# Kernel optimization log

Measured on AMD Instinct MI355X. Metric: run time of the kernel, lower is better.

## Reference

```python
import jax, jax.numpy as jnp
import numpy as np

B, T, D, H = 4, 2048, 1024, 16
HD = D // H  # head_dim = 64

def setup_inputs() -> dict:
    key = jax.random.key(0)
    k1, k2, k3 = jax.random.split(key, 3)
    s = 1.0 / np.sqrt(D)
    x = jax.random.normal(k1, (B, T, D), dtype=jnp.float32)
    W_qkv = jax.random.normal(k2, (D, 3 * D), dtype=jnp.float32) * s
    W_proj = jax.random.normal(k3, (D, D), dtype=jnp.float32) * s
    return {"x": x, "W_qkv": W_qkv, "W_proj": W_proj}

def reference(x, W_qkv, W_proj):
    Bq, Tq, C = x.shape
    qkv = x @ W_qkv                                   # [B,T,3C]
    q, k, v = jnp.split(qkv, 3, axis=-1)
    def heads(t):  # [B,T,C] -> [B,H,T,HD]
        return t.reshape(Bq, Tq, H, HD).transpose(0, 2, 1, 3)
    q, k, v = heads(q), heads(k), heads(v)
    scale = 1.0 / np.sqrt(HD)
    att = jnp.einsum('bhqd,bhkd->bhqk', q, k) * scale  # [B,H,T,T]
    causal = jnp.tril(jnp.ones((Tq, Tq), dtype=bool))
    att = jnp.where(causal[None, None], att, -jnp.inf)
    att = jax.nn.softmax(att, axis=-1)
    y = jnp.einsum('bhqk,bhkd->bhqd', att, v)          # [B,H,T,HD]
    y = y.transpose(0, 2, 1, 3).reshape(Bq, Tq, C)
    return y @ W_proj
```

## Files before the change

kernel.cpp:

```cpp
#include <hip/hip_runtime.h>

typedef unsigned short ushort_t;
typedef __attribute__((ext_vector_type(8))) __bf16 bf16x8;
typedef __attribute__((ext_vector_type(4))) float f32x4;
typedef __attribute__((ext_vector_type(16))) float f32x16;
typedef __attribute__((ext_vector_type(4))) float float4v;
typedef __attribute__((ext_vector_type(8))) unsigned short ushort8v;
typedef __attribute__((ext_vector_type(4))) unsigned short ushort4v;
typedef __attribute__((ext_vector_type(4))) unsigned uint4v;

#define T_LEN 2048
#define D_DIM 1024
#define NHEAD 16
#define HDIM 64
#define BH 64
#define MROWS 8192
#define PERQKV ((size_t)BH * T_LEN * HDIM)

__device__ __forceinline__ ushort_t f2bf(float f) {
  unsigned u = __builtin_bit_cast(unsigned, f);
  u = (u + 0x7FFFu + ((u >> 16) & 1u)) >> 16;
  return (ushort_t)u;
}

__device__ __forceinline__ float fast_exp2(float x) {
  float r; asm("v_exp_f32 %0, %1" : "=v"(r) : "v"(x)); return r;
}

__device__ __forceinline__ void load_lds16(const ushort_t* g, ushort_t* l) {
  __builtin_amdgcn_global_load_lds((const __attribute__((address_space(1))) void*)g,
                                   (__attribute__((address_space(3))) void*)l, 16, 0, 0);
}

__global__ __launch_bounds__(256) void k_cvt_x(const float* __restrict__ x,
                                               ushort_t* __restrict__ xb) {
  int i = blockIdx.x * 256 + threadIdx.x;
  float4v v = ((const float4v*)x)[i];
  ushort4v o;
  o[0] = f2bf(v[0]); o[1] = f2bf(v[1]); o[2] = f2bf(v[2]); o[3] = f2bf(v[3]);
  ((ushort4v*)xb)[i] = o;
}

__global__ __launch_bounds__(256) void k_transpose(const float* __restrict__ W,
                                                   ushort_t* __restrict__ Wt,
                                                   int R, int C) {
  __shared__ ushort_t tile[32][33];
  int tx = threadIdx.x & 31, ty = threadIdx.x >> 5;
  int r0 = blockIdx.y << 5, c0 = blockIdx.x << 5;
#pragma unroll
  for (int i = 0; i < 4; ++i) {
    int r = ty + i * 8;
    tile[r][tx] = f2bf(W[(size_t)(r0 + r) * C + c0 + tx]);
  }
  __syncthreads();
#pragma unroll
  for (int i = 0; i < 4; ++i) {
    int r = ty + i * 8;
    Wt[(size_t)(c0 + r) * R + r0 + tx] = tile[tx][r];
  }
}

template <int N, int K, int EPI>
__global__ __launch_bounds__(256) void k_gemm(const ushort_t* __restrict__ A,
                                              const ushort_t* __restrict__ Bt,
                                              ushort_t* __restrict__ O16,
                                              float* __restrict__ O32) {
  __shared__ __align__(16) ushort_t Atile[128 * 32];
  __shared__ __align__(16) ushort_t Btile[128 * 32];
  const int tid = threadIdx.x;
  const int lane = tid & 63, w = tid >> 6;
  const int g = lane >> 4, c = lane & 15;
  const int wm = w >> 1, wn = w & 1;
  const int m0 = blockIdx.y * 128, n0 = blockIdx.x * 128;

  f32x4 acc[4][4];
#pragma unroll
  for (int i = 0; i < 4; ++i)
#pragma unroll
    for (int j = 0; j < 4; ++j) acc[i][j] = (f32x4){0.f, 0.f, 0.f, 0.f};

  for (int k0 = 0; k0 < K; k0 += 32) {
    __syncthreads();
#pragma unroll
    for (int r = 0; r < 2; ++r) {
      int flat = r * 256 + tid;
      int row = flat >> 2, slot = flat & 3;
      int gsl = slot ^ (row & 3);
      load_lds16(A + (size_t)(m0 + row) * K + k0 + gsl * 8,
                 &Atile[(r * 256 + w * 64) * 8]);
      load_lds16(Bt + (size_t)(n0 + row) * K + k0 + gsl * 8,
                 &Btile[(r * 256 + w * 64) * 8]);
    }
    __syncthreads();

    bf16x8 af[4], bfr[4];
#pragma unroll
    for (int mi = 0; mi < 4; ++mi) {
      int row = wm * 64 + mi * 16 + c;
      int sl = g ^ (row & 3);
      af[mi] = *(const bf16x8*)&Atile[row * 32 + sl * 8];
    }
#pragma unroll
    for (int ni = 0; ni < 4; ++ni) {
      int row = wn * 64 + ni * 16 + c;
      int sl = g ^ (row & 3);
      bfr[ni] = *(const bf16x8*)&Btile[row * 32 + sl * 8];
    }
#pragma unroll
    for (int mi = 0; mi < 4; ++mi)
#pragma unroll
      for (int ni = 0; ni < 4; ++ni)
        acc[mi][ni] = __builtin_amdgcn_mfma_f32_16x16x32_bf16(af[mi], bfr[ni],
                                                              acc[mi][ni], 0, 0, 0);
  }

#pragma unroll
  for (int mi = 0; mi < 4; ++mi)
#pragma unroll
    for (int ni = 0; ni < 4; ++ni) {
      int n = n0 + wn * 64 + ni * 16 + c;
#pragma unroll
      for (int j = 0; j < 4; ++j) {
        int m = m0 + wm * 64 + mi * 16 + g * 4 + j;
        float v = acc[mi][ni][j];
        if constexpr (EPI == 0) {
          int which = n >> 10, hn = n & 1023;
          int h = hn >> 6, d = hn & 63;
          int b = m >> 11, t = m & 2047;
          if (which == 0) v *= 0.18033688f;
          O16[(size_t)which * PERQKV +
              (((size_t)(b * NHEAD + h) * T_LEN + t) * HDIM + d)] = f2bf(v);
        } else {
          O32[(size_t)m * N + n] = v;
        }
      }
    }
}

__global__ __launch_bounds__(128, 4) void k_attn(const ushort_t* __restrict__ Q,
                                                 const ushort_t* __restrict__ Kv,
                                                 const ushort_t* __restrict__ Vv,
                                                 ushort_t* __restrict__ Y) {
  __shared__ __align__(16) ushort_t Kt[2][64 * 64];
  __shared__ __align__(16) ushort_t Vt[2][64 * 64];

  const int bid = blockIdx.x;
  const int bh = (bid & 7) * 8 + ((bid >> 3) & 7);
  const int pairidx = bid >> 6;
  const int pA = 31 - pairidx, pB = pairidx;
  const int nktA = pA + 1;
  const int total = nktA + pB + 1;

  const int tid = threadIdx.x, lane = tid & 63, w = tid >> 6;
  const int hi = lane >> 5, lc = lane & 31;
  const size_t base = (size_t)bh * (T_LEN * HDIM);

  int q32 = pA * 64 + w * 32;
  bf16x8 qf[4];
#pragma unroll
  for (int st = 0; st < 4; ++st)
    qf[st] = *(const bf16x8*)(Q + base + (size_t)(q32 + lc) * HDIM + st * 16 + hi * 8);

  f32x16 o0, o1;
#pragma unroll
  for (int i = 0; i < 16; ++i) { o0[i] = 0.f; o1[i] = 0.f; }
  float mrun = 0.f, lrun = 0.f;

  const int ksl = tid & 7, krow0 = tid >> 3;
  const int kpair = tid & 31, vk0 = 2 * kpair, vd0 = (tid >> 5) * 8;

  bf16x8 kreg[4];
  ushort8v vreg[4];
  auto stage_issue = [&](int kt) {
    const ushort_t* kb = Kv + base + (size_t)kt * 64 * HDIM;
    const ushort_t* vb = Vv + base + (size_t)kt * 64 * HDIM;
    vreg[0] = *(const ushort8v*)(vb + (size_t)vk0 * HDIM + vd0);
    vreg[1] = *(const ushort8v*)(vb + (size_t)(vk0 + 1) * HDIM + vd0);
    vreg[2] = *(const ushort8v*)(vb + (size_t)vk0 * HDIM + vd0 + 32);
    vreg[3] = *(const ushort8v*)(vb + (size_t)(vk0 + 1) * HDIM + vd0 + 32);
#pragma unroll
    for (int m = 0; m < 4; ++m)
      kreg[m] = *(const bf16x8*)(kb + (size_t)(krow0 + 16 * m) * HDIM + ksl * 8);
  };
  auto stage_write = [&](int buf) {
#pragma unroll
    for (int m = 0; m < 4; ++m) {
      int r = krow0 + 16 * m;
      *(bf16x8*)&Kt[buf][r * 64 + ((ksl ^ (r & 7)) << 3)] = kreg[m];
    }
#pragma unroll
    for (int e = 0; e < 8; ++e) {
      int rd = vd0 + e;
      unsigned pv = (unsigned)vreg[0][e] | ((unsigned)vreg[1][e] << 16);
      *(unsigned*)&Vt[buf][rd * 64 + (((kpair >> 2) ^ (rd & 7)) << 3) + 2 * (kpair & 3)] = pv;
      int rd2 = rd + 32;
      unsigned pv2 = (unsigned)vreg[2][e] | ((unsigned)vreg[3][e] << 16);
      *(unsigned*)&Vt[buf][rd2 * 64 + (((kpair >> 2) ^ (rd2 & 7)) << 3) + 2 * (kpair & 3)] = pv2;
    }
  };

  const int b_ = bh >> 4, h_ = bh & 15;
  auto epilogue = [&]() {
    float lt = lrun + __shfl_xor(lrun, 32);
    float invl = 1.f / lt;
#pragma unroll
    for (int r = 0; r < 16; ++r) {
      int cr = (r & 3) + 8 * (r >> 2) + 4 * hi;
      float iv = __shfl(invl, cr);
      size_t m = (size_t)b_ * T_LEN + q32 + cr;
      Y[m * D_DIM + h_ * HDIM + lc]      = f2bf(o0[r] * iv);
      Y[m * D_DIM + h_ * HDIM + 32 + lc] = f2bf(o1[r] * iv);
    }
  };

  stage_issue(0); stage_write(0);
  stage_issue(1);
  __syncthreads();

  for (int it = 0; it < total; ++it) {
    if (it == nktA) {
      epilogue();
      q32 = pB * 64 + w * 32;
#pragma unroll
      for (int st = 0; st < 4; ++st)
        qf[st] = *(const bf16x8*)(Q + base + (size_t)(q32 + lc) * HDIM + st * 16 + hi * 8);
#pragma unroll
      for (int i = 0; i < 16; ++i) { o0[i] = 0.f; o1[i] = 0.f; }
      mrun = 0.f; lrun = 0.f;
    }
    const int kt = (it < nktA) ? it : it - nktA;
    const int cur = it & 1;
    const ushort_t* kbuf = &Kt[cur][0];
    const ushort_t* vbuf = &Vt[cur][0];

    f32x16 s0, s1;
#pragma unroll
    for (int i = 0; i < 16; ++i) { s0[i] = 0.f; s1[i] = 0.f; }
    __builtin_amdgcn_s_setprio(1);
#pragma unroll
    for (int st = 0; st < 4; ++st) {
      bf16x8 kf0 = *(const bf16x8*)&kbuf[lc * 64 + (((2 * st + hi) ^ (lc & 7)) << 3)];
      s0 = __builtin_amdgcn_mfma_f32_32x32x16_bf16(kf0, qf[st], s0, 0, 0, 0);
    }
#pragma unroll
    for (int st = 0; st < 4; ++st) {
      bf16x8 kf1 = *(const bf16x8*)&kbuf[(32 + lc) * 64 + (((2 * st + hi) ^ (lc & 7)) << 3)];
      s1 = __builtin_amdgcn_mfma_f32_32x32x16_bf16(kf1, qf[st], s1, 0, 0, 0);
    }
    __builtin_amdgcn_s_setprio(0);

    if (kt * 64 + 63 > q32) {
      const int q = q32 + lc;
#pragma unroll
      for (int r = 0; r < 16; ++r) {
        int cr = (r & 3) + 8 * (r >> 2) + 4 * hi;
        if (kt * 64 + cr > q)      s0[r] = -3.0e38f;
        if (kt * 64 + 32 + cr > q) s1[r] = -3.0e38f;
      }
    }

    float tm[8];
#pragma unroll
    for (int i = 0; i < 8; ++i) tm[i] = fmaxf(fmaxf(s0[i], s0[i + 8]), fmaxf(s1[i], s1[i + 8]));
#pragma unroll
    for (int i = 0; i < 4; ++i) tm[i] = fmaxf(tm[i], tm[i + 4]);
    float tmax = fmaxf(fmaxf(tm[0], tm[1]), fmaxf(tm[2], tm[3]));
    tmax = fmaxf(tmax, __shfl_xor(tmax, 32));

    if (!__all(tmax <= mrun + 11.0f)) {
      float mnew = fmaxf(mrun, tmax);
      float sc = fast_exp2(mrun - mnew);
      lrun *= sc; mrun = mnew;
#pragma unroll
      for (int r = 0; r < 16; ++r) {
        int cr = (r & 3) + 8 * (r >> 2) + 4 * hi;
        float scr = __shfl(sc, cr);
        o0[r] *= scr; o1[r] *= scr;
      }
    }

#pragma unroll
    for (int r = 0; r < 16; ++r) s0[r] = fast_exp2(s0[r] - mrun);
#pragma unroll
    for (int r = 0; r < 16; ++r) s1[r] = fast_exp2(s1[r] - mrun);
    {
      float u0 = 0.f, u1 = 0.f, u2 = 0.f, u3 = 0.f;
#pragma unroll
      for (int i = 0; i < 4; ++i) {
        u0 += s0[i];     u1 += s0[i + 4];  u2 += s0[i + 8];  u3 += s0[i + 12];
        u0 += s1[i];     u1 += s1[i + 4];  u2 += s1[i + 8];  u3 += s1[i + 12];
      }
      lrun += (u0 + u1) + (u2 + u3);
    }

    unsigned wv[16];
#pragma unroll
    for (int i = 0; i < 8; ++i) {
      asm("v_cvt_pk_bf16_f32 %0, %1, %2" : "=v"(wv[i])     : "v"(s0[2 * i]), "v"(s0[2 * i + 1]));
      asm("v_cvt_pk_bf16_f32 %0, %1, %2" : "=v"(wv[8 + i]) : "v"(s1[2 * i]), "v"(s1[2 * i + 1]));
    }
    bf16x8 pf[4];
#pragma unroll
    for (int g4 = 0; g4 < 4; ++g4) {
      unsigned a0 = wv[4 * g4], a1 = wv[4 * g4 + 1];
      unsigned a2 = wv[4 * g4 + 2], a3 = wv[4 * g4 + 3];
      asm("v_permlane32_swap_b32 %0, %1" : "+v"(a0), "+v"(a2));
      asm("v_permlane32_swap_b32 %0, %1" : "+v"(a1), "+v"(a3));
      uint4v fw; fw[0] = a0; fw[1] = a1; fw[2] = a2; fw[3] = a3;
      pf[g4] = __builtin_bit_cast(bf16x8, fw);
    }

    __builtin_amdgcn_s_setprio(1);
#pragma unroll
    for (int km = 0; km < 4; ++km) {
      int gsl = ((2 * km + hi) ^ (lc & 7)) << 3;
      bf16x8 vb0 = *(const bf16x8*)&vbuf[lc * 64 + gsl];
      bf16x8 vb1 = *(const bf16x8*)&vbuf[(32 + lc) * 64 + gsl];
      o0 = __builtin_amdgcn_mfma_f32_32x32x16_bf16(pf[km], vb0, o0, 0, 0, 0);
      o1 = __builtin_amdgcn_mfma_f32_32x32x16_bf16(pf[km], vb1, o1, 0, 0, 0);
    }
    __builtin_amdgcn_s_setprio(0);

    if (it + 1 < total) stage_write((it + 1) & 1);
    if (it + 2 < total) {
      int itn = it + 2;
      stage_issue((itn < nktA) ? itn : itn - nktA);
    }
    __syncthreads();
  }

  epilogue();
}

extern "C" void kernel_launch(void* const* d_in, const int* in_sizes, int n_in,
                              void* d_out, int out_size, void* d_ws, size_t ws_size,
                              hipStream_t stream) {
  const float* x     = (const float*)d_in[0];
  const float* Wqkv  = (const float*)d_in[1];
  const float* Wproj = (const float*)d_in[2];
  float* out = (float*)d_out;
  ushort_t* ws = (ushort_t*)d_ws;

  ushort_t* Xb  = ws;
  ushort_t* WqT = Xb  + (size_t)MROWS * D_DIM;
  ushort_t* WpT = WqT + (size_t)3 * D_DIM * D_DIM;
  ushort_t* Qb  = WpT + (size_t)D_DIM * D_DIM;
  ushort_t* Kb  = Qb + PERQKV;
  ushort_t* Vb  = Kb + PERQKV;
  ushort_t* Yb  = Vb + PERQKV;

  k_cvt_x<<<(MROWS * D_DIM / 4) / 256, 256, 0, stream>>>(x, Xb);
  k_transpose<<<dim3(3 * D_DIM / 32, D_DIM / 32), 256, 0, stream>>>(Wqkv, WqT, D_DIM, 3 * D_DIM);
  k_transpose<<<dim3(D_DIM / 32, D_DIM / 32), 256, 0, stream>>>(Wproj, WpT, D_DIM, D_DIM);
  k_gemm<3 * D_DIM, D_DIM, 0><<<dim3(3 * D_DIM / 128, MROWS / 128), 256, 0, stream>>>(Xb, WqT, Qb, nullptr);
  k_attn<<<1024, 128, 0, stream>>>(Qb, Kb, Vb, Yb);
  k_gemm<D_DIM, D_DIM, 1><<<dim3(D_DIM / 128, MROWS / 128), 256, 0, stream>>>(Yb, WpT, nullptr, out);
}
```

Baseline: 189.1 us.

## Add larger-tile double-buffered QKV GEMM with swizzled LDS and XCD-aware block mapping

Replaces the 128x128 QKV projection GEMM with a dedicated 256x192-tile kernel using 512 threads, K-step of 64, double-buffered direct-to-LDS loads, XOR-swizzled shared-memory layout, and a block-index remap that groups tiles per XCD. It also raises MFMA issue priority around the compute loop. The goal is higher arithmetic intensity and overlap of global loads with MFMA work. The cost is heavier register and LDS use (two 80 KB-ish buffers), which may limit occupancy.

```diff
diff --git a/kernel.cpp b/kernel.cpp
--- a/kernel.cpp
+++ b/kernel.cpp
@@ -58,6 +58,94 @@
     int r = ty + i * 8;
     Wt[(size_t)(c0 + r) * R + r0 + tx] = tile[tx][r];
   }
+}
+
+__global__ __launch_bounds__(512, 2) void k_gemm1(const ushort_t* __restrict__ A,
+                                                  const ushort_t* __restrict__ Bt,
+                                                  ushort_t* __restrict__ O16) {
+  __shared__ __align__(16) ushort_t As[2][256 * 64];
+  __shared__ __align__(16) ushort_t Bs[2][192 * 64];
+  const int tid = threadIdx.x, lane = tid & 63, w = tid >> 6;
+  const int g = lane >> 4, c = lane & 15;
+  const int wm = w & 1, wn = w >> 1;
+  const int bid = blockIdx.x;
+  const int logical = (bid & 7) * 64 + (bid >> 3);
+  const int mb = logical & 31, nb = logical >> 5;
+  const int m0 = mb * 256, n0 = nb * 192;
+
+  const int strow = w * 8 + (lane >> 3);
+  const int stslot = lane & 7;
+
+  auto stage = [&](int t, int buf) {
+    const int k0 = t * 64;
+#pragma unroll
+    for (int i = 0; i < 4; ++i) {
+      int row = i * 64 + strow;
+      load_lds16(A + (size_t)(m0 + row) * 1024 + k0 + ((stslot ^ (row & 7)) << 3),
+                 &As[buf][(i * 512 + w * 64) * 8]);
+    }
+#pragma unroll
+    for (int i = 0; i < 3; ++i) {
+      int row = i * 64 + strow;
+      load_lds16(Bt + (size_t)(n0 + row) * 1024 + k0 + ((stslot ^ (row & 7)) << 3),
+                 &Bs[buf][(i * 512 + w * 64) * 8]);
+    }
+  };
+
+  f32x4 acc[8][3];
+#pragma unroll
+  for (int fr = 0; fr < 8; ++fr)
+#pragma unroll
+    for (int fc = 0; fc < 3; ++fc) acc[fr][fc] = (f32x4){0.f, 0.f, 0.f, 0.f};
+
+  stage(0, 0);
+  __syncthreads();
+
+  for (int t = 0; t < 16; ++t) {
+    if (t + 1 < 16) stage(t + 1, (t + 1) & 1);
+    const int cur = t & 1;
+#pragma unroll
+    for (int kk = 0; kk < 2; ++kk) {
+      bf16x8 af[8], bfr[3];
+#pragma unroll
+      for (int fr = 0; fr < 8; ++fr) {
+        int r = wm * 128 + fr * 16 + c;
+        af[fr] = *(const bf16x8*)&As[cur][r * 64 + (((kk * 4 + g) ^ (r & 7)) << 3)];
+      }
+#pragma unroll
+      for (int fc = 0; fc < 3; ++fc) {
+        int r = wn * 48 + fc * 16 + c;
+        bfr[fc] = *(const bf16x8*)&Bs[cur][r * 64 + (((kk * 4 + g) ^ (r & 7)) << 3)];
+      }
+      __builtin_amdgcn_s_setprio(1);
+#pragma unroll
+      for (int fr = 0; fr < 8; ++fr)
+#pragma unroll
+        for (int fc = 0; fc < 3; ++fc)
+          acc[fr][fc] = __builtin_amdgcn_mfma_f32_16x16x32_bf16(af[fr], bfr[fc],
+                                                                acc[fr][fc], 0, 0, 0);
+      __builtin_amdgcn_s_setprio(0);
+    }
+    __syncthreads();
+  }
+
+#pragma unroll
+  for (int fr = 0; fr < 8; ++fr)
+#pragma unroll
+    for (int fc = 0; fc < 3; ++fc) {
+      int n = n0 + wn * 48 + fc * 16 + c;
+      int which = n >> 10, hn = n & 1023;
+      int h = hn >> 6, d = hn & 63;
+#pragma unroll
+      for (int j = 0; j < 4; ++j) {
+        int m = m0 + wm * 128 + fr * 16 + g * 4 + j;
+        float v = acc[fr][fc][j];
+        int b = m >> 11, tt = m & 2047;
+        if (which == 0) v *= 0.18033688f;
+        O16[(size_t)which * PERQKV +
+            (((size_t)(b * NHEAD + h) * T_LEN + tt) * HDIM + d)] = f2bf(v);
+      }
+    }
 }
 
 template <int N, int K, int EPI>
@@ -352,7 +440,7 @@
   k_cvt_x<<<(MROWS * D_DIM / 4) / 256, 256, 0, stream>>>(x, Xb);
   k_transpose<<<dim3(3 * D_DIM / 32, D_DIM / 32), 256, 0, stream>>>(Wqkv, WqT, D_DIM, 3 * D_DIM);
   k_transpose<<<dim3(D_DIM / 32, D_DIM / 32), 256, 0, stream>>>(Wproj, WpT, D_DIM, D_DIM);
-  k_gemm<3 * D_DIM, D_DIM, 0><<<dim3(3 * D_DIM / 128, MROWS / 128), 256, 0, stream>>>(Xb, WqT, Qb, nullptr);
+  k_gemm1<<<512, 512, 0, stream>>>(Xb, WqT, Qb);
   k_attn<<<1024, 128, 0, stream>>>(Qb, Kb, Vb, Yb);
   k_gemm<D_DIM, D_DIM, 1><<<dim3(D_DIM / 128, MROWS / 128), 256, 0, stream>>>(Yb, WpT, nullptr, out);
 }
```

Measured after the change: 190.7 us. Within noise of the previous version (+0.8%).

## Rewrite projection GEMMs with 128x256 tiles and triple-buffered async LDS pipeline

Applied to the files above, without the earlier changes.

Replaces the single-buffered 128x128 GEMM with a 512-thread kernel using 128x256 tiles, K-step 64, and a three-stage LDS ring filled by async global-to-LDS loads, with waits via explicit vmcnt counts. Blocks are remapped in chunks across the XCDs for L2 locality, and MFMA sections are raised in priority with s_setprio. This is meant to hide global load latency and reduce barrier stalls in the QKV and output projections. In exchange it uses much more LDS per block (about 144KB), which limits occupancy, and relies on hand-counted vmcnt values that must match the number of loads issued.

```diff
diff --git a/kernel.cpp b/kernel.cpp
--- a/kernel.cpp
+++ b/kernel.cpp
@@ -60,18 +60,40 @@
   }
 }
 
-template <int N, int K, int EPI>
-__global__ __launch_bounds__(256) void k_gemm(const ushort_t* __restrict__ A,
-                                              const ushort_t* __restrict__ Bt,
-                                              ushort_t* __restrict__ O16,
-                                              float* __restrict__ O32) {
-  __shared__ __align__(16) ushort_t Atile[128 * 32];
-  __shared__ __align__(16) ushort_t Btile[128 * 32];
-  const int tid = threadIdx.x;
-  const int lane = tid & 63, w = tid >> 6;
+template <int NB_TILES, int EPI>
+__global__ __launch_bounds__(512, 2) void k_gemm3(const ushort_t* __restrict__ A,
+                                                  const ushort_t* __restrict__ Bt,
+                                                  ushort_t* __restrict__ O16,
+                                                  float* __restrict__ O32) {
+  __shared__ __align__(16) ushort_t As[3][128 * 64];
+  __shared__ __align__(16) ushort_t Bs[3][256 * 64];
+  const int tid = threadIdx.x, lane = tid & 63, w = tid >> 6;
   const int g = lane >> 4, c = lane & 15;
-  const int wm = w >> 1, wn = w & 1;
-  const int m0 = blockIdx.y * 128, n0 = blockIdx.x * 128;
+  const int wm = w & 1, wn = w >> 1;
+  const int nblk = 64 * NB_TILES;
+  const int chunk = nblk >> 3;
+  const int bid = blockIdx.x;
+  const int logical = (bid & 7) * chunk + (bid >> 3);
+  const int mb = logical & 63, nb = logical >> 6;
+  const int m0 = mb * 128, n0 = nb * 256;
+
+  const int srow = lane >> 3, sgran = lane & 7;
+
+  auto stage = [&](int t, int buf) {
+    const int k0 = t * 64;
+#pragma unroll
+    for (int l = 0; l < 2; ++l) {
+      int r = w * 16 + l * 8 + srow;
+      load_lds16(A + (size_t)(m0 + r) * 1024 + k0 + ((sgran ^ (r & 7)) << 3),
+                 &As[buf][(w * 16 + l * 8) * 64]);
+    }
+#pragma unroll
+    for (int l = 0; l < 4; ++l) {
+      int r = w * 32 + l * 8 + srow;
+      load_lds16(Bt + (size_t)(n0 + r) * 1024 + k0 + ((sgran ^ (r & 7)) << 3),
+                 &Bs[buf][(w * 32 + l * 8) * 64]);
+    }
+  };
 
   f32x4 acc[4][4];
 #pragma unroll
@@ -79,59 +101,62 @@
 #pragma unroll
     for (int j = 0; j < 4; ++j) acc[i][j] = (f32x4){0.f, 0.f, 0.f, 0.f};
 
-  for (int k0 = 0; k0 < K; k0 += 32) {
-    __syncthreads();
-#pragma unroll
-    for (int r = 0; r < 2; ++r) {
-      int flat = r * 256 + tid;
-      int row = flat >> 2, slot = flat & 3;
-      int gsl = slot ^ (row & 3);
-      load_lds16(A + (size_t)(m0 + row) * K + k0 + gsl * 8,
-                 &Atile[(r * 256 + w * 64) * 8]);
-      load_lds16(Bt + (size_t)(n0 + row) * K + k0 + gsl * 8,
-                 &Btile[(r * 256 + w * 64) * 8]);
-    }
-    __syncthreads();
-
-    bf16x8 af[4], bfr[4];
-#pragma unroll
-    for (int mi = 0; mi < 4; ++mi) {
-      int row = wm * 64 + mi * 16 + c;
-      int sl = g ^ (row & 3);
-      af[mi] = *(const bf16x8*)&Atile[row * 32 + sl * 8];
-    }
-#pragma unroll
-    for (int ni = 0; ni < 4; ++ni) {
-      int row = wn * 64 + ni * 16 + c;
-      int sl = g ^ (row & 3);
-      bfr[ni] = *(const bf16x8*)&Btile[row * 32 + sl * 8];
-    }
-#pragma unroll
-    for (int mi = 0; mi < 4; ++mi)
-#pragma unroll
-      for (int ni = 0; ni < 4; ++ni)
-        acc[mi][ni] = __builtin_amdgcn_mfma_f32_16x16x32_bf16(af[mi], bfr[ni],
-                                                              acc[mi][ni], 0, 0, 0);
+  stage(0, 0);
+  stage(1, 1);
+
+  for (int t = 0; t < 16; ++t) {
+    if (t < 15) asm volatile("s_waitcnt vmcnt(6)" ::: "memory");
+    else        asm volatile("s_waitcnt vmcnt(0)" ::: "memory");
+    __builtin_amdgcn_s_barrier();
+    __builtin_amdgcn_sched_barrier(0);
+
+    if (t + 2 < 16) stage(t + 2, (t + 2) % 3);
+
+    const int cur = t % 3;
+    const ushort_t* abuf = &As[cur][0];
+    const ushort_t* bbuf = &Bs[cur][0];
+#pragma unroll
+    for (int kk = 0; kk < 2; ++kk) {
+      bf16x8 af[4], bq[4];
+#pragma unroll
+      for (int fr = 0; fr < 4; ++fr) {
+        int r = wm * 64 + fr * 16 + c;
+        af[fr] = *(const bf16x8*)&abuf[r * 64 + (((kk * 4 + g) ^ (r & 7)) << 3)];
+      }
+#pragma unroll
+      for (int fc = 0; fc < 4; ++fc) {
+        int r = wn * 64 + fc * 16 + c;
+        bq[fc] = *(const bf16x8*)&bbuf[r * 64 + (((kk * 4 + g) ^ (r & 7)) << 3)];
+      }
+      __builtin_amdgcn_s_setprio(1);
+#pragma unroll
+      for (int fr = 0; fr < 4; ++fr)
+#pragma unroll
+        for (int fc = 0; fc < 4; ++fc)
+          acc[fr][fc] = __builtin_amdgcn_mfma_f32_16x16x32_bf16(af[fr], bq[fc],
+                                                                acc[fr][fc], 0, 0, 0);
+      __builtin_amdgcn_s_setprio(0);
+    }
   }
 
 #pragma unroll
-  for (int mi = 0; mi < 4; ++mi)
-#pragma unroll
-    for (int ni = 0; ni < 4; ++ni) {
-      int n = n0 + wn * 64 + ni * 16 + c;
+  for (int fr = 0; fr < 4; ++fr)
+#pragma unroll
+    for (int fc = 0; fc < 4; ++fc) {
+      int n = n0 + wn * 64 + fc * 16 + c;
 #pragma unroll
       for (int j = 0; j < 4; ++j) {
-        int m = m0 + wm * 64 + mi * 16 + g * 4 + j;
-        float v = acc[mi][ni][j];
+        int m = m0 + wm * 64 + fr * 16 + g * 4 + j;
+        float v = acc[fr][fc][j];
         if constexpr (EPI == 0) {
           int which = n >> 10, hn = n & 1023;
           int h = hn >> 6, d = hn & 63;
-          int b = m >> 11, t = m & 2047;
+          int b = m >> 11, tt = m & 2047;
           if (which == 0) v *= 0.18033688f;
           O16[(size_t)which * PERQKV +
-              (((size_t)(b * NHEAD + h) * T_LEN + t) * HDIM + d)] = f2bf(v);
+              (((size_t)(b * NHEAD + h) * T_LEN + tt) * HDIM + d)] = f2bf(v);
         } else {
-          O32[(size_t)m * N + n] = v;
+          O32[(size_t)m * (64 * NB_TILES * 4) + n] = v;
         }
       }
     }
@@ -352,7 +377,7 @@
   k_cvt_x<<<(MROWS * D_DIM / 4) / 256, 256, 0, stream>>>(x, Xb);
   k_transpose<<<dim3(3 * D_DIM / 32, D_DIM / 32), 256, 0, stream>>>(Wqkv, WqT, D_DIM, 3 * D_DIM);
   k_transpose<<<dim3(D_DIM / 32, D_DIM / 32), 256, 0, stream>>>(Wproj, WpT, D_DIM, D_DIM);
-  k_gemm<3 * D_DIM, D_DIM, 0><<<dim3(3 * D_DIM / 128, MROWS / 128), 256, 0, stream>>>(Xb, WqT, Qb, nullptr);
+  k_gemm3<12, 0><<<768, 512, 0, stream>>>(Xb, WqT, Qb, nullptr);
   k_attn<<<1024, 128, 0, stream>>>(Qb, Kb, Vb, Yb);
-  k_gemm<D_DIM, D_DIM, 1><<<dim3(D_DIM / 128, MROWS / 128), 256, 0, stream>>>(Yb, WpT, nullptr, out);
-}
+  k_gemm3<4, 1><<<256, 512, 0, stream>>>(Yb, WpT, nullptr, out);
+}
```

New measurement: 195.6 us. 1.03x slower.
